# Optimization experiments

Hardware: AMD Instinct MI355X
Metric: run time of the kernel (lower is better)

Reference implementation:

```python
import jax, jax.numpy as jnp
import numpy as np

D_MODEL = 1024
HIDDEN = 64


def setup_inputs() -> dict:
    key = jax.random.key(0)
    ks = jax.random.split(key, 11)
    B, N = 8, 4096
    scale_in = 1.0 / np.sqrt(D_MODEL)
    scale_h = 1.0 / np.sqrt(HIDDEN)
    return {
        "query": jax.random.normal(ks[0], (B, N, D_MODEL), jnp.float32),
        "key": jax.random.normal(ks[1], (B, N, D_MODEL), jnp.float32),
        "value": jax.random.normal(ks[2], (B, N, D_MODEL), jnp.float32),
        # torch nn.Linear(d_model, 64): weight [64, d_model], bias [64]
        "Wq": jax.random.uniform(ks[3], (HIDDEN, D_MODEL), jnp.float32, -scale_in, scale_in),
        "bq": jax.random.uniform(ks[4], (HIDDEN,), jnp.float32, -scale_in, scale_in),
        "Wk": jax.random.uniform(ks[5], (HIDDEN, D_MODEL), jnp.float32, -scale_in, scale_in),
        "bk": jax.random.uniform(ks[6], (HIDDEN,), jnp.float32, -scale_in, scale_in),
        "Wv": jax.random.uniform(ks[7], (HIDDEN, D_MODEL), jnp.float32, -scale_in, scale_in),
        "bv": jax.random.uniform(ks[8], (HIDDEN,), jnp.float32, -scale_in, scale_in),
        # project: nn.Linear(64, d_model): weight [d_model, 64], bias [d_model]
        "Wp": jax.random.uniform(ks[9], (D_MODEL, HIDDEN), jnp.float32, -scale_h, scale_h),
        "bp": jax.random.uniform(ks[10], (D_MODEL,), jnp.float32, -scale_h, scale_h),
    }


def reference(query, key, value, Wq, bq, Wk, bk, Wv, bv, Wp, bp):
    # q/k/v projections: [B, N, d_model] -> [B, N, 64]
    q = jnp.einsum('bnd,hd->bnh', query, Wq) + bq
    k = jnp.einsum('bnd,hd->bnh', key, Wk) + bk
    v = jnp.einsum('bnd,hd->bnh', value, Wv) + bv
    # softmax over sequence dim (dim=1), weighted pool over sequence -> [B, 1, 64]
    attn = jax.nn.softmax(k, axis=1)
    weights = jnp.sum(attn * v, axis=1, keepdims=True)
    # gated broadcast: sigmoid(q) * pooled weights -> [B, N, 64]
    Yt = jax.nn.sigmoid(q) * weights
    # project back: [B, N, 64] -> [B, N, d_model]
    return jnp.einsum('bnh,dh->bnd', Yt, Wp) + bp
```

## Files before the change

### kernel.cpp

```cpp
#include <hip/hip_runtime.h>
#include <hip/hip_bf16.h>

#define BB 8
#define NN 4096
#define DD 1024
#define HH 64

typedef __bf16 bf8v __attribute__((ext_vector_type(8)));
typedef __bf16 bf4v __attribute__((ext_vector_type(4)));
typedef float  f4v  __attribute__((ext_vector_type(4)));
typedef __hip_bfloat16 bf16;

__device__ __forceinline__ f4v mfma16x16x32(bf8v a, bf8v b, f4v c) {
    return __builtin_amdgcn_mfma_f32_16x16x32_bf16(a, b, c, 0, 0, 0);
}

__device__ __forceinline__ bf8v cvt8(const float* p) {
    const f4v a = ((const f4v*)p)[0];
    const f4v b = ((const f4v*)p)[1];
    bf8v r;
    #pragma unroll
    for (int i = 0; i < 4; ++i) { r[i] = (__bf16)a[i]; r[i + 4] = (__bf16)b[i]; }
    return r;
}

__device__ __forceinline__ bf8v ldg8(const bf16* p) {
    return *(const bf8v*)p;
}

__global__ __launch_bounds__(256) void convert_weights_kernel(
    const float* __restrict__ Wq, const float* __restrict__ Wk,
    const float* __restrict__ Wv, const float* __restrict__ Wp,
    bf16* __restrict__ cw)
{
    const int idx = blockIdx.x * 256 + threadIdx.x;
    const int t = idx >> 14;
    const int e = (idx & 16383) * 4;
    const float* src = (t == 0) ? Wq : (t == 1) ? Wk : (t == 2) ? Wv : Wp;
    f4v x = *(const f4v*)(src + e);
    bf4v r;
    #pragma unroll
    for (int i = 0; i < 4; ++i) r[i] = (__bf16)x[i];
    *(bf4v*)(cw + t * 65536 + e) = r;
}

__global__ __launch_bounds__(256) void kv_reduce_kernel(
    const float* __restrict__ key, const float* __restrict__ value,
    const bf16* __restrict__ cWk, const float* __restrict__ bk,
    const bf16* __restrict__ cWv, const float* __restrict__ bv,
    float* __restrict__ se, float* __restrict__ sev)
{
    const int lane = threadIdx.x & 63;
    const int wave = threadIdx.x >> 6;
    const int cl   = lane & 15;
    const int quad = lane >> 4;
    const int b     = blockIdx.x >> 6;
    const int chunk = blockIdx.x & 63;
    const int row   = chunk * 64 + wave * 16 + cl;

    const float* kp = key   + ((size_t)b * NN + row) * DD + quad * 8;
    const float* vp = value + ((size_t)b * NN + row) * DD + quad * 8;
    const bf16* wk = cWk + (size_t)cl * DD + quad * 8;
    const bf16* wv = cWv + (size_t)cl * DD + quad * 8;

    f4v kacc[4], vacc[4];
    #pragma unroll
    for (int i = 0; i < 4; ++i) {
        kacc[i] = (f4v){0.f, 0.f, 0.f, 0.f};
        vacc[i] = (f4v){0.f, 0.f, 0.f, 0.f};
    }

    #pragma unroll 4
    for (int k0 = 0; k0 < DD; k0 += 32) {
        bf8v ak = cvt8(kp + k0);
        bf8v av = cvt8(vp + k0);
        #pragma unroll
        for (int ht = 0; ht < 4; ++ht) {
            bf8v bk8 = ldg8(wk + (size_t)ht * 16 * DD + k0);
            bf8v bv8 = ldg8(wv + (size_t)ht * 16 * DD + k0);
            kacc[ht] = mfma16x16x32(ak, bk8, kacc[ht]);
            vacc[ht] = mfma16x16x32(av, bv8, vacc[ht]);
        }
    }

    #pragma unroll
    for (int ht = 0; ht < 4; ++ht) {
        const int h = ht * 16 + cl;
        const float bkh = bk[h];
        const float bvh = bv[h];
        float sep = 0.f, sevp = 0.f;
        #pragma unroll
        for (int r = 0; r < 4; ++r) {
            float e = __expf(kacc[ht][r] + bkh);
            sep  += e;
            sevp += e * (vacc[ht][r] + bvh);
        }
        sep  += __shfl_xor(sep, 16, 64);
        sevp += __shfl_xor(sevp, 16, 64);
        sep  += __shfl_xor(sep, 32, 64);
        sevp += __shfl_xor(sevp, 32, 64);
        if (quad == 0) {
            atomicAdd(&se[b * HH + h], sep);
            atomicAdd(&sev[b * HH + h], sevp);
        }
    }
}

__global__ __launch_bounds__(256) void out_kernel(
    const float* __restrict__ query,
    const bf16* __restrict__ cWq, const float* __restrict__ bq,
    const bf16* __restrict__ cWp, const float* __restrict__ bp,
    const float* __restrict__ se, const float* __restrict__ sev,
    float* __restrict__ out)
{
    __shared__ __align__(16) bf16 gsh[4][16][72];

    const int lane = threadIdx.x & 63;
    const int wave = threadIdx.x >> 6;
    const int cl   = lane & 15;
    const int quad = lane >> 4;
    const int b     = blockIdx.x >> 6;
    const int chunk = blockIdx.x & 63;
    const int row0  = chunk * 64 + wave * 16;

    f4v qacc[4];
    #pragma unroll
    for (int i = 0; i < 4; ++i) qacc[i] = (f4v){0.f, 0.f, 0.f, 0.f};

    const float* qp = query + ((size_t)b * NN + row0 + cl) * DD + quad * 8;
    const bf16*  wq = cWq + (size_t)cl * DD + quad * 8;

    #pragma unroll 4
    for (int k0 = 0; k0 < DD; k0 += 32) {
        bf8v aq = cvt8(qp + k0);
        #pragma unroll
        for (int ht = 0; ht < 4; ++ht) {
            bf8v bw = ldg8(wq + (size_t)ht * 16 * DD + k0);
            qacc[ht] = mfma16x16x32(aq, bw, qacc[ht]);
        }
    }

    #pragma unroll
    for (int ht = 0; ht < 4; ++ht) {
        const int h = ht * 16 + cl;
        const float w   = sev[b * HH + h] / se[b * HH + h];
        const float bqh = bq[h];
        #pragma unroll
        for (int r = 0; r < 4; ++r) {
            float q = qacc[ht][r] + bqh;
            float s = 1.0f / (1.0f + __expf(-q));
            gsh[wave][quad * 4 + r][h] = __float2bfloat16(s * w);
        }
    }
    __syncthreads();

    bf8v a2[2];
    #pragma unroll
    for (int kk = 0; kk < 2; ++kk)
        a2[kk] = *(const bf8v*)&gsh[wave][cl][kk * 32 + quad * 8];

    const bf16* wp = cWp + (size_t)cl * HH + quad * 8;
    const size_t outbase = ((size_t)b * NN + row0 + quad * 4) * DD;

    #pragma unroll 4
    for (int nt = 0; nt < 64; ++nt) {
        const int d0 = nt * 16;
        f4v o = (f4v){0.f, 0.f, 0.f, 0.f};
        o = mfma16x16x32(a2[0], ldg8(wp + (size_t)d0 * HH), o);
        o = mfma16x16x32(a2[1], ldg8(wp + (size_t)d0 * HH + 32), o);
        const int dcol = d0 + cl;
        const float bpd = bp[dcol];
        #pragma unroll
        for (int r = 0; r < 4; ++r) {
            out[outbase + (size_t)r * DD + dcol] = o[r] + bpd;
        }
    }
}

extern "C" void kernel_launch(void* const* d_in, const int* in_sizes, int n_in,
                              void* d_out, int out_size, void* d_ws, size_t ws_size,
                              hipStream_t stream)
{
    const float* query = (const float*)d_in[0];
    const float* key_  = (const float*)d_in[1];
    const float* value = (const float*)d_in[2];
    const float* Wq = (const float*)d_in[3];
    const float* bq = (const float*)d_in[4];
    const float* Wk = (const float*)d_in[5];
    const float* bk = (const float*)d_in[6];
    const float* Wv = (const float*)d_in[7];
    const float* bv = (const float*)d_in[8];
    const float* Wp = (const float*)d_in[9];
    const float* bp = (const float*)d_in[10];
    float* out = (float*)d_out;

    float* se  = (float*)d_ws;
    float* sev = se + BB * HH;
    bf16*  cw  = (bf16*)((char*)d_ws + 4096);

    hipMemsetAsync(d_ws, 0, 2 * BB * HH * sizeof(float), stream);

    convert_weights_kernel<<<dim3(256), dim3(256), 0, stream>>>(Wq, Wk, Wv, Wp, cw);
    kv_reduce_kernel<<<dim3(512), dim3(256), 0, stream>>>(
        key_, value, cw + 1 * 65536, bk, cw + 2 * 65536, bv, se, sev);
    out_kernel<<<dim3(512), dim3(256), 0, stream>>>(
        query, cw + 0 * 65536, bq, cw + 3 * 65536, bp, se, sev, out);
}
```

Baseline: 507.8 us.

## Fuse Q/K/V projections into one kernel and materialize sigmoid gate

Moves the query projection into the same kernel as the key/value reduction, with interleaved blocks for the two roles. The kernel stores sigmoid(q) into a gate buffer in the workspace. Work is split across more, smaller blocks, and global loads are software-prefetched one step ahead. The output kernel now reads the gate, scales it by the pooled weights and splits the projection columns across waves. The aim is to stream query, key and value in one concurrent pass and raise occupancy, at the cost of an extra 8 MB gate write and read.

```diff
diff --git a/kernel.cpp b/kernel.cpp
--- a/kernel.cpp
+++ b/kernel.cpp
@@ -15,18 +15,14 @@
     return __builtin_amdgcn_mfma_f32_16x16x32_bf16(a, b, c, 0, 0, 0);
 }
 
-__device__ __forceinline__ bf8v cvt8(const float* p) {
-    const f4v a = ((const f4v*)p)[0];
-    const f4v b = ((const f4v*)p)[1];
+__device__ __forceinline__ bf8v pack8(f4v a, f4v b) {
     bf8v r;
     #pragma unroll
     for (int i = 0; i < 4; ++i) { r[i] = (__bf16)a[i]; r[i + 4] = (__bf16)b[i]; }
     return r;
 }
 
-__device__ __forceinline__ bf8v ldg8(const bf16* p) {
-    return *(const bf8v*)p;
-}
+__device__ __forceinline__ bf8v ldg8(const bf16* p) { return *(const bf8v*)p; }
 
 __global__ __launch_bounds__(256) void convert_weights_kernel(
     const float* __restrict__ Wq, const float* __restrict__ Wk,
@@ -44,136 +40,172 @@
     *(bf4v*)(cw + t * 65536 + e) = r;
 }
 
-__global__ __launch_bounds__(256) void kv_reduce_kernel(
-    const float* __restrict__ key, const float* __restrict__ value,
-    const bf16* __restrict__ cWk, const float* __restrict__ bk,
-    const bf16* __restrict__ cWv, const float* __restrict__ bv,
-    float* __restrict__ se, float* __restrict__ sev)
+__global__ __launch_bounds__(256, 4) void proj_kernel(
+    const float* __restrict__ query, const float* __restrict__ key,
+    const float* __restrict__ value, const bf16* __restrict__ cw,
+    const float* __restrict__ bq, const float* __restrict__ bk,
+    const float* __restrict__ bv,
+    float* __restrict__ se, float* __restrict__ sev,
+    float* __restrict__ gate)
+{
+    const int lane  = threadIdx.x & 63;
+    const int wave  = threadIdx.x >> 6;
+    const int cl    = lane & 15;
+    const int quad  = lane >> 4;
+    const int rhalf = wave >> 1;
+    const int hhalf = wave & 1;
+    const int is_q  = blockIdx.x & 1;
+    const int bid   = blockIdx.x >> 1;
+    const int b     = bid >> 7;
+    const int chunk = bid & 127;
+    const int row0  = chunk * 32 + rhalf * 16;
+
+    const size_t abase = ((size_t)b * NN + row0 + cl) * DD + quad * 8;
+    const size_t wbase = (size_t)(hhalf * 32 + cl) * DD + quad * 8;
+
+    if (is_q) {
+        const float* qp = query + abase;
+        const bf16*  wq = cw + wbase;
+
+        f4v qacc[2];
+        qacc[0] = qacc[1] = (f4v){0.f, 0.f, 0.f, 0.f};
+
+        f4v a0 = *(const f4v*)qp, a1 = *(const f4v*)(qp + 4);
+        bf8v w0 = ldg8(wq), w1 = ldg8(wq + 16 * DD);
+
+        #pragma unroll
+        for (int s = 0; s < 32; ++s) {
+            f4v na0, na1; bf8v nw0, nw1;
+            if (s < 31) {
+                const int k0 = (s + 1) * 32;
+                na0 = *(const f4v*)(qp + k0); na1 = *(const f4v*)(qp + k0 + 4);
+                nw0 = ldg8(wq + k0);          nw1 = ldg8(wq + 16 * DD + k0);
+            }
+            bf8v aq = pack8(a0, a1);
+            qacc[0] = mfma16x16x32(aq, w0, qacc[0]);
+            qacc[1] = mfma16x16x32(aq, w1, qacc[1]);
+            if (s < 31) { a0 = na0; a1 = na1; w0 = nw0; w1 = nw1; }
+        }
+
+        const size_t gbase = ((size_t)b * NN + row0 + quad * 4) * HH;
+        #pragma unroll
+        for (int t2 = 0; t2 < 2; ++t2) {
+            const int h = hhalf * 32 + t2 * 16 + cl;
+            const float bqh = bq[h];
+            #pragma unroll
+            for (int r = 0; r < 4; ++r) {
+                float qv = qacc[t2][r] + bqh;
+                float sg = 1.0f / (1.0f + __expf(-qv));
+                gate[gbase + (size_t)r * HH + h] = sg;
+            }
+        }
+    } else {
+        const float* kp = key   + abase;
+        const float* vp = value + abase;
+        const bf16*  wk = cw + 1 * 65536 + wbase;
+        const bf16*  wv = cw + 2 * 65536 + wbase;
+
+        f4v kacc[2], vacc[2];
+        kacc[0] = kacc[1] = vacc[0] = vacc[1] = (f4v){0.f, 0.f, 0.f, 0.f};
+
+        f4v ka0 = *(const f4v*)kp, ka1 = *(const f4v*)(kp + 4);
+        f4v va0 = *(const f4v*)vp, va1 = *(const f4v*)(vp + 4);
+        bf8v wk0 = ldg8(wk), wk1 = ldg8(wk + 16 * DD);
+        bf8v wv0 = ldg8(wv), wv1 = ldg8(wv + 16 * DD);
+
+        #pragma unroll
+        for (int s = 0; s < 32; ++s) {
+            f4v nka0, nka1, nva0, nva1;
+            bf8v nwk0, nwk1, nwv0, nwv1;
+            if (s < 31) {
+                const int k0 = (s + 1) * 32;
+                nka0 = *(const f4v*)(kp + k0); nka1 = *(const f4v*)(kp + k0 + 4);
+                nva0 = *(const f4v*)(vp + k0); nva1 = *(const f4v*)(vp + k0 + 4);
+                nwk0 = ldg8(wk + k0);          nwk1 = ldg8(wk + 16 * DD + k0);
+                nwv0 = ldg8(wv + k0);          nwv1 = ldg8(wv + 16 * DD + k0);
+            }
+            bf8v ak = pack8(ka0, ka1);
+            bf8v av = pack8(va0, va1);
+            kacc[0] = mfma16x16x32(ak, wk0, kacc[0]);
+            kacc[1] = mfma16x16x32(ak, wk1, kacc[1]);
+            vacc[0] = mfma16x16x32(av, wv0, vacc[0]);
+            vacc[1] = mfma16x16x32(av, wv1, vacc[1]);
+            if (s < 31) {
+                ka0 = nka0; ka1 = nka1; va0 = nva0; va1 = nva1;
+                wk0 = nwk0; wk1 = nwk1; wv0 = nwv0; wv1 = nwv1;
+            }
+        }
+
+        #pragma unroll
+        for (int t2 = 0; t2 < 2; ++t2) {
+            const int h = hhalf * 32 + t2 * 16 + cl;
+            const float bkh = bk[h];
+            const float bvh = bv[h];
+            float sep = 0.f, sevp = 0.f;
+            #pragma unroll
+            for (int r = 0; r < 4; ++r) {
+                float e = __expf(kacc[t2][r] + bkh);
+                sep  += e;
+                sevp += e * (vacc[t2][r] + bvh);
+            }
+            sep  += __shfl_xor(sep, 16, 64);
+            sevp += __shfl_xor(sevp, 16, 64);
+            sep  += __shfl_xor(sep, 32, 64);
+            sevp += __shfl_xor(sevp, 32, 64);
+            if (quad == 0) {
+                atomicAdd(&se[b * HH + h], sep);
+                atomicAdd(&sev[b * HH + h], sevp);
+            }
+        }
+    }
+}
+
+__global__ __launch_bounds__(256) void out_kernel(
+    const float* __restrict__ gate, const bf16* __restrict__ cWp,
+    const float* __restrict__ bp, const float* __restrict__ se,
+    const float* __restrict__ sev, float* __restrict__ out)
 {
     const int lane = threadIdx.x & 63;
     const int wave = threadIdx.x >> 6;
     const int cl   = lane & 15;
     const int quad = lane >> 4;
-    const int b     = blockIdx.x >> 6;
-    const int chunk = blockIdx.x & 63;
-    const int row   = chunk * 64 + wave * 16 + cl;
-
-    const float* kp = key   + ((size_t)b * NN + row) * DD + quad * 8;
-    const float* vp = value + ((size_t)b * NN + row) * DD + quad * 8;
-    const bf16* wk = cWk + (size_t)cl * DD + quad * 8;
-    const bf16* wv = cWv + (size_t)cl * DD + quad * 8;
-
-    f4v kacc[4], vacc[4];
-    #pragma unroll
-    for (int i = 0; i < 4; ++i) {
-        kacc[i] = (f4v){0.f, 0.f, 0.f, 0.f};
-        vacc[i] = (f4v){0.f, 0.f, 0.f, 0.f};
-    }
-
-    #pragma unroll 4
-    for (int k0 = 0; k0 < DD; k0 += 32) {
-        bf8v ak = cvt8(kp + k0);
-        bf8v av = cvt8(vp + k0);
-        #pragma unroll
-        for (int ht = 0; ht < 4; ++ht) {
-            bf8v bk8 = ldg8(wk + (size_t)ht * 16 * DD + k0);
-            bf8v bv8 = ldg8(wv + (size_t)ht * 16 * DD + k0);
-            kacc[ht] = mfma16x16x32(ak, bk8, kacc[ht]);
-            vacc[ht] = mfma16x16x32(av, bv8, vacc[ht]);
-        }
-    }
-
-    #pragma unroll
-    for (int ht = 0; ht < 4; ++ht) {
-        const int h = ht * 16 + cl;
-        const float bkh = bk[h];
-        const float bvh = bv[h];
-        float sep = 0.f, sevp = 0.f;
-        #pragma unroll
-        for (int r = 0; r < 4; ++r) {
-            float e = __expf(kacc[ht][r] + bkh);
-            sep  += e;
-            sevp += e * (vacc[ht][r] + bvh);
-        }
-        sep  += __shfl_xor(sep, 16, 64);
-        sevp += __shfl_xor(sevp, 16, 64);
-        sep  += __shfl_xor(sep, 32, 64);
-        sevp += __shfl_xor(sevp, 32, 64);
-        if (quad == 0) {
-            atomicAdd(&se[b * HH + h], sep);
-            atomicAdd(&sev[b * HH + h], sevp);
-        }
-    }
-}
-
-__global__ __launch_bounds__(256) void out_kernel(
-    const float* __restrict__ query,
-    const bf16* __restrict__ cWq, const float* __restrict__ bq,
-    const bf16* __restrict__ cWp, const float* __restrict__ bp,
-    const float* __restrict__ se, const float* __restrict__ sev,
-    float* __restrict__ out)
-{
-    __shared__ __align__(16) bf16 gsh[4][16][72];
-
-    const int lane = threadIdx.x & 63;
-    const int wave = threadIdx.x >> 6;
-    const int cl   = lane & 15;
-    const int quad = lane >> 4;
-    const int b     = blockIdx.x >> 6;
-    const int chunk = blockIdx.x & 63;
-    const int row0  = chunk * 64 + wave * 16;
-
-    f4v qacc[4];
-    #pragma unroll
-    for (int i = 0; i < 4; ++i) qacc[i] = (f4v){0.f, 0.f, 0.f, 0.f};
-
-    const float* qp = query + ((size_t)b * NN + row0 + cl) * DD + quad * 8;
-    const bf16*  wq = cWq + (size_t)cl * DD + quad * 8;
-
-    #pragma unroll 4
-    for (int k0 = 0; k0 < DD; k0 += 32) {
-        bf8v aq = cvt8(qp + k0);
-        #pragma unroll
-        for (int ht = 0; ht < 4; ++ht) {
-            bf8v bw = ldg8(wq + (size_t)ht * 16 * DD + k0);
-            qacc[ht] = mfma16x16x32(aq, bw, qacc[ht]);
-        }
-    }
-
-    #pragma unroll
-    for (int ht = 0; ht < 4; ++ht) {
-        const int h = ht * 16 + cl;
-        const float w   = sev[b * HH + h] / se[b * HH + h];
-        const float bqh = bq[h];
-        #pragma unroll
-        for (int r = 0; r < 4; ++r) {
-            float q = qacc[ht][r] + bqh;
-            float s = 1.0f / (1.0f + __expf(-q));
-            gsh[wave][quad * 4 + r][h] = __float2bfloat16(s * w);
-        }
-    }
-    __syncthreads();
+    const int b     = blockIdx.x >> 8;
+    const int chunk = blockIdx.x & 255;
+    const int row0  = chunk * 16;
+
+    const float* gp = gate + ((size_t)b * NN + row0 + cl) * HH + quad * 8;
 
     bf8v a2[2];
     #pragma unroll
-    for (int kk = 0; kk < 2; ++kk)
-        a2[kk] = *(const bf8v*)&gsh[wave][cl][kk * 32 + quad * 8];
+    for (int kk = 0; kk < 2; ++kk) {
+        f4v g0 = *(const f4v*)(gp + kk * 32);
+        f4v g1 = *(const f4v*)(gp + kk * 32 + 4);
+        const int hb = kk * 32 + quad * 8;
+        f4v s0 = *(const f4v*)(se  + b * HH + hb);
+        f4v s1 = *(const f4v*)(se  + b * HH + hb + 4);
+        f4v v0 = *(const f4v*)(sev + b * HH + hb);
+        f4v v1 = *(const f4v*)(sev + b * HH + hb + 4);
+        #pragma unroll
+        for (int j = 0; j < 4; ++j) {
+            a2[kk][j]     = (__bf16)(g0[j] * __fdividef(v0[j], s0[j]));
+            a2[kk][j + 4] = (__bf16)(g1[j] * __fdividef(v1[j], s1[j]));
+        }
+    }
 
     const bf16* wp = cWp + (size_t)cl * HH + quad * 8;
     const size_t outbase = ((size_t)b * NN + row0 + quad * 4) * DD;
 
     #pragma unroll 4
-    for (int nt = 0; nt < 64; ++nt) {
-        const int d0 = nt * 16;
+    for (int nt = 0; nt < 16; ++nt) {
+        const int d0 = wave * 256 + nt * 16;
         f4v o = (f4v){0.f, 0.f, 0.f, 0.f};
         o = mfma16x16x32(a2[0], ldg8(wp + (size_t)d0 * HH), o);
         o = mfma16x16x32(a2[1], ldg8(wp + (size_t)d0 * HH + 32), o);
         const int dcol = d0 + cl;
         const float bpd = bp[dcol];
         #pragma unroll
-        for (int r = 0; r < 4; ++r) {
+        for (int r = 0; r < 4; ++r)
             out[outbase + (size_t)r * DD + dcol] = o[r] + bpd;
-        }
     }
 }
 
@@ -194,15 +226,16 @@
     const float* bp = (const float*)d_in[10];
     float* out = (float*)d_out;
 
-    float* se  = (float*)d_ws;
-    float* sev = se + BB * HH;
-    bf16*  cw  = (bf16*)((char*)d_ws + 4096);
+    float* se   = (float*)d_ws;
+    float* sev  = se + BB * HH;
+    bf16*  cw   = (bf16*)((char*)d_ws + 4096);
+    float* gate = (float*)((char*)d_ws + 4096 + 4 * 65536 * sizeof(bf16));
 
     hipMemsetAsync(d_ws, 0, 2 * BB * HH * sizeof(float), stream);
 
     convert_weights_kernel<<<dim3(256), dim3(256), 0, stream>>>(Wq, Wk, Wv, Wp, cw);
-    kv_reduce_kernel<<<dim3(512), dim3(256), 0, stream>>>(
-        key_, value, cw + 1 * 65536, bk, cw + 2 * 65536, bv, se, sev);
-    out_kernel<<<dim3(512), dim3(256), 0, stream>>>(
-        query, cw + 0 * 65536, bq, cw + 3 * 65536, bp, se, sev, out);
-}
+    proj_kernel<<<dim3(2048), dim3(256), 0, stream>>>(
+        query, key_, value, cw, bq, bk, bv, se, sev, gate);
+    out_kernel<<<dim3(2048), dim3(256), 0, stream>>>(
+        gate, cw + 3 * 65536, bp, se, sev, out);
+}
```

After: 613.8 us. 20.9% more time.
